# Kernel optimization log

Measured on AMD Instinct MI355X. Metric: run time of the kernel, lower is better.

The kernel has to match this reference:

```python
import jax, jax.numpy as jnp
import numpy as np

N_NODES = 50000
N_EDGES = 800000
IN_DIM = 256     # state_size
HID = 256        # hidden_dim
ACT = 64         # action_size


def gcn_conv(x, src, dst, norm, W, b):
    # PyG GCNConv: out[dst] += norm_e * (x @ W)[src]; then + bias
    h = x @ W                               # [N, out]
    msg = h[src] * norm[:, None]            # [E+N, out]
    agg = jax.ops.segment_sum(msg, dst, num_segments=N_NODES)
    return agg + b


def gcn_norm(edge_index):
    # add self-loops, symmetric normalization deg^-1/2[src]*deg^-1/2[dst]
    loops = jnp.arange(N_NODES, dtype=edge_index.dtype)
    src = jnp.concatenate([edge_index[0], loops])
    dst = jnp.concatenate([edge_index[1], loops])
    deg = jax.ops.segment_sum(jnp.ones_like(dst, dtype=jnp.float32), dst,
                              num_segments=N_NODES)
    dinv = jnp.where(deg > 0, jax.lax.rsqrt(deg), 0.0)
    norm = dinv[src] * dinv[dst]            # [E+N]
    return src, dst, norm


def setup_inputs() -> dict:
    key = jax.random.key(0)
    ks = jax.random.split(key, 12)
    x = jax.random.normal(ks[0], (N_NODES, IN_DIM), dtype=jnp.float32)
    edge_index = jax.random.randint(ks[1], (2, N_EDGES), 0, N_NODES, dtype=jnp.int64)

    def glorot(k, shape):
        lim = float(np.sqrt(6.0 / (shape[0] + shape[1])))
        return jax.random.uniform(k, shape, jnp.float32, -lim, lim)

    return {
        "x": x, "edge_index": edge_index,
        "W1": glorot(ks[2], (IN_DIM, HID)), "b1": jnp.zeros((HID,), jnp.float32),
        "W2": glorot(ks[3], (HID, HID)),    "b2": jnp.zeros((HID,), jnp.float32),
        "fcW1": glorot(ks[4], (HID, HID)),  "fcb1": jnp.zeros((HID,), jnp.float32),
        "fcW2": glorot(ks[5], (HID, HID)),  "fcb2": jnp.zeros((HID,), jnp.float32),
        "fcW3": glorot(ks[6], (HID, ACT)),  "fcb3": jnp.zeros((ACT,), jnp.float32),
    }


def reference(x, edge_index, W1, b1, W2, b2, fcW1, fcb1, fcW2, fcb2, fcW3, fcb3):
    src, dst, norm = gcn_norm(edge_index)
    h = jax.nn.relu(gcn_conv(x, src, dst, norm, W1, b1))   # GNNLayer 1
    h = jax.nn.relu(gcn_conv(h, src, dst, norm, W2, b2))   # GNNLayer 2
    g = jax.nn.relu(jnp.mean(h, axis=0)[None, :])          # [1, HID]
    g = jax.nn.relu(g @ fcW1 + fcb1)
    g = jax.nn.relu(g @ fcW2 + fcb2)
    return g @ fcW3 + fcb3                                 # [1, ACT]
```

## Files before the change

### kernel.cpp

```cpp
#include <hip/hip_runtime.h>

#define N_NODES 50000
#define N_EDGES 800000
#define DIM 256
#define ACT 64
#define SCAN_B 256
#define SCAN_NB ((N_NODES + SCAN_B - 1) / SCAN_B)
#define SLICE_ELEMS ((size_t)N_NODES * 32)
#define AGG_CHUNKS 512
#define TOTAL_GROUPS (AGG_CHUNKS * 32)
#define CSR_MAX (N_EDGES + 16 * N_NODES + 64)
#define NBINS 16
#define NBB (NBINS * SCAN_NB)

typedef __attribute__((ext_vector_type(8))) short short8_t;
typedef __attribute__((ext_vector_type(4))) float f32x4;
typedef __attribute__((ext_vector_type(4))) unsigned short ushort4_t;

__device__ __forceinline__ unsigned short f2b(float x) {
    unsigned u = __float_as_uint(x);
    unsigned r = u + 0x7FFFu + ((u >> 16) & 1u);
    return (unsigned short)(r >> 16);
}

__device__ __forceinline__ int deg_bin_desc(int deg) {
    int rounds = ((deg + 16) & ~15) >> 4;
    if (rounds > NBINS - 1) rounds = NBINS - 1;
    return (NBINS - 1) - rounds;
}


__global__ __launch_bounds__(256) void k_cvt_wt2(const float* __restrict__ W1,
                                                 const float* __restrict__ W2,
                                                 unsigned short* __restrict__ W1t,
                                                 unsigned short* __restrict__ W2t) {
    int b = blockIdx.x;
    const float* W = (b < 256) ? W1 : W2;
    unsigned short* Wt = (b < 256) ? W1t : W2t;
    int i = (b & 255) * 256 + threadIdx.x;
    int k = i >> 8, n = i & 255;
    Wt[n * DIM + k] = f2b(W[k * DIM + n]);
}


__global__ void k_deg_count(const int* __restrict__ ei, int* degi) {
    int e = blockIdx.x * blockDim.x + threadIdx.x;
    if (e < N_EDGES) atomicAdd(&degi[ei[N_EDGES + e]], 1);
}


__global__ __launch_bounds__(256) void k_hist_rank(const int* __restrict__ degi,
                                                   int* blockbin,
                                                   unsigned char* lrank) {
    __shared__ int lh[NBINS];
    int t = threadIdx.x;
    if (t < NBINS) lh[t] = 0;
    __syncthreads();
    int i = blockIdx.x * 256 + t;
    if (i < N_NODES) {
        int bin = deg_bin_desc(degi[i]);
        lrank[i] = (unsigned char)atomicAdd(&lh[bin], 1);
    }
    __syncthreads();
    if (t < NBINS) blockbin[t * SCAN_NB + blockIdx.x] = lh[t];
}

__global__ __launch_bounds__(256) void k_scan_bins(const int* __restrict__ blockbin,
                                                   int* blockbase) {
    __shared__ int sm[256];
    int t = threadIdx.x;
    const int CH = (NBB + 255) / 256;
    int s0 = t * CH;
    int s1 = s0 + CH; if (s1 > NBB) s1 = NBB;
    int s = 0;
    for (int i = s0; i < s1; ++i) s += blockbin[i];
    sm[t] = s;
    __syncthreads();
#pragma unroll
    for (int off = 1; off < 256; off <<= 1) {
        int u = (t >= off) ? sm[t - off] : 0;
        __syncthreads();
        sm[t] += u;
        __syncthreads();
    }
    int base = sm[t] - s;
    for (int i = s0; i < s1; ++i) { int v = blockbin[i]; blockbase[i] = base; base += v; }
}

__global__ __launch_bounds__(256) void k_perm_apply(const int* __restrict__ degi,
                                                    const int* __restrict__ blockbase,
                                                    const unsigned char* __restrict__ lrank,
                                                    int* perm) {
    int i = blockIdx.x * 256 + threadIdx.x;
    if (i >= N_NODES) return;
    int bin = deg_bin_desc(degi[i]);
    perm[blockbase[bin * SCAN_NB + blockIdx.x] + lrank[i]] = i;
}


__global__ __launch_bounds__(SCAN_B) void k_scan_local(const int* __restrict__ degi,
                                                       const int* __restrict__ perm,
                                                       int* lexc, int* btot) {
    __shared__ int sm[SCAN_B];
    int t = threadIdx.x;
    int i = blockIdx.x * SCAN_B + t;
    int v = (i < N_NODES) ? ((degi[perm[i]] + 16) & ~15) : 0;
    sm[t] = v;
    __syncthreads();
#pragma unroll
    for (int off = 1; off < SCAN_B; off <<= 1) {
        int u = (t >= off) ? sm[t - off] : 0;
        __syncthreads();
        sm[t] += u;
        __syncthreads();
    }
    if (i < N_NODES) lexc[i] = sm[t] - v;
    if (t == SCAN_B - 1) btot[blockIdx.x] = sm[t];
}

__global__ __launch_bounds__(SCAN_B) void k_scan_tops(const int* __restrict__ btot,
                                                      int* bbase, int* rowstart) {
    __shared__ int sm[SCAN_B];
    int t = threadIdx.x;
    int v = (t < SCAN_NB) ? btot[t] : 0;
    sm[t] = v;
    __syncthreads();
#pragma unroll
    for (int off = 1; off < SCAN_B; off <<= 1) {
        int u = (t >= off) ? sm[t - off] : 0;
        __syncthreads();
        sm[t] += u;
        __syncthreads();
    }
    if (t < SCAN_NB) bbase[t] = sm[t] - v;
    if (t == SCAN_NB - 1) rowstart[N_NODES] = sm[t];
}

__global__ __launch_bounds__(SCAN_B) void k_scan_apply(const int* __restrict__ degi,
                                                       const int* __restrict__ perm,
                                                       const int* __restrict__ lexc,
                                                       const int* __restrict__ bbase,
                                                       int* rowstart, int* fillpos,
                                                       float* dinv, unsigned* csr4) {
    int i = blockIdx.x * SCAN_B + threadIdx.x;
    if (i >= N_NODES) return;
    int rs = bbase[blockIdx.x] + lexc[i];
    rowstart[i] = rs;
    int n = perm[i];
    int d = degi[n] + 1;
    float di = rsqrtf((float)d);
    dinv[n] = di;
    csr4[rs] = ((unsigned)n << 16) | f2b(di * di);
    fillpos[n] = rs + 1;
}

__global__ void k_fill_edge(const int* __restrict__ ei,
                            const float* __restrict__ dinv, int* fillpos,
                            unsigned* csr4) {
    int e = blockIdx.x * blockDim.x + threadIdx.x;
    if (e < N_EDGES) {
        int s = ei[e];
        int d = ei[N_EDGES + e];
        int p = atomicAdd(&fillpos[d], 1);
        csr4[p] = ((unsigned)s << 16) | f2b(dinv[s] * dinv[d]);
    }
}


template <int AFP32>
__global__ __launch_bounds__(512) void k_gemm_mfma(const void* __restrict__ Ap,
                                                   const unsigned short* __restrict__ Wt,
                                                   unsigned short* __restrict__ H,
                                                   int M) {
    __shared__ char lds[49152];
    char* AsB = lds;
    char* BsB = lds + 16384;

    int tid = threadIdx.x;
    int w = tid >> 6;
    int l = tid & 63;
    int wr = w >> 2, wc = w & 3;
    int r0 = blockIdx.x * 128;

    f32x4 acc[4][4];
#pragma unroll
    for (int i = 0; i < 4; ++i)
#pragma unroll
        for (int j = 0; j < 4; ++j) acc[i][j] = (f32x4)(0.f);

    for (int kt = 0; kt < 4; ++kt) {
        int k0 = kt * 64;
#pragma unroll
        for (int i = 0; i < 2; ++i) {
            int c = tid + i * 512;
            int row = c >> 3, kc = c & 7;
            int gg = r0 + row; if (gg >= M) gg = M - 1;
            short8_t v;
            if (AFP32) {
                const float* A = (const float*)Ap;
                const float4* src = (const float4*)(A + (size_t)gg * DIM + k0 + kc * 8);
                float4 f0 = src[0], f1 = src[1];
                v[0] = (short)f2b(f0.x); v[1] = (short)f2b(f0.y);
                v[2] = (short)f2b(f0.z); v[3] = (short)f2b(f0.w);
                v[4] = (short)f2b(f1.x); v[5] = (short)f2b(f1.y);
                v[6] = (short)f2b(f1.z); v[7] = (short)f2b(f1.w);
            } else {
                const unsigned short* A = (const unsigned short*)Ap;
                int k = k0 + kc * 8;
                int slice = k >> 5, within = k & 31;
                v = *(const short8_t*)(A + (size_t)slice * SLICE_ELEMS + (size_t)gg * 32 + within);
            }
            int off = (row * 128 + kc * 16) ^ ((row & 7) << 4);
            *(short8_t*)(AsB + off) = v;
        }
#pragma unroll
        for (int i = 0; i < 4; ++i) {
            int c = tid + i * 512;
            int n = c >> 3, kc = c & 7;
            short8_t v = *(const short8_t*)(Wt + n * DIM + k0 + kc * 8);
            int off = (n * 128 + kc * 16) ^ ((n & 7) << 4);
            *(short8_t*)(BsB + off) = v;
        }
        __syncthreads();

#pragma unroll
        for (int kf = 0; kf < 2; ++kf) {
            int kb = kf * 64 + (l >> 4) * 16;
            short8_t a[4], b[4];
#pragma unroll
            for (int fm = 0; fm < 4; ++fm) {
                int ra = wr * 64 + fm * 16 + (l & 15);
                a[fm] = *(const short8_t*)(AsB + ((ra * 128 + kb) ^ ((ra & 7) << 4)));
            }
#pragma unroll
            for (int fn = 0; fn < 4; ++fn) {
                int nb = wc * 64 + fn * 16 + (l & 15);
                b[fn] = *(const short8_t*)(BsB + ((nb * 128 + kb) ^ ((nb & 7) << 4)));
            }
#pragma unroll
            for (int fm = 0; fm < 4; ++fm)
#pragma unroll
                for (int fn = 0; fn < 4; ++fn)
                    acc[fm][fn] = __builtin_amdgcn_mfma_f32_16x16x32_bf16(
                        a[fm], b[fn], acc[fm][fn], 0, 0, 0);
        }
        __syncthreads();
    }

#pragma unroll
    for (int fm = 0; fm < 4; ++fm) {
#pragma unroll
        for (int i = 0; i < 4; ++i) {
            int row = r0 + wr * 64 + fm * 16 + ((l >> 4) << 2) + i;
            if (row >= M) continue;
#pragma unroll
            for (int fn = 0; fn < 4; ++fn) {
                int col = wc * 64 + fn * 16 + (l & 15);
                int slice = col >> 5;
                H[(size_t)slice * SLICE_ELEMS + (size_t)row * 32 + (col & 31)] = f2b(acc[fm][fn][i]);
            }
        }
    }
}


__global__ __launch_bounds__(256) void k_agg_sliced(const unsigned short* __restrict__ H,
                                                    const int* __restrict__ rowstart,
                                                    const unsigned* __restrict__ csr4,
                                                    const int* __restrict__ perm,
                                                    const float* __restrict__ bias,
                                                    unsigned short* __restrict__ X,
                                                    float* __restrict__ gsum,
                                                    int write_out) {
    __shared__ unsigned pbuf[32 * 68];
    int slice = blockIdx.x & 7;
    int chunk = blockIdx.x >> 3;
    int g = threadIdx.x >> 3;
    int lane = threadIdx.x & 7;
    const char* Hb = (const char*)(H + (size_t)slice * SLICE_ELEMS) + (lane << 3);
    unsigned short* Xs = X + (size_t)slice * SLICE_ELEMS;
    int d0 = slice * 32 + lane * 4;
    float4 bb = *(const float4*)&bias[d0];
    float c0 = 0.f, c1 = 0.f, c2 = 0.f, c3 = 0.f;
    unsigned* ps = pbuf + g * 68;
    int fg = chunk * 32 + g;
    for (int idx = fg; idx < N_NODES; idx += TOTAL_GROUPS) {
        int n = perm[idx];
        int beg = rowstart[idx], end = rowstart[idx + 1];
        float a0 = 0.f, a1 = 0.f, a2 = 0.f, a3 = 0.f;
        uint4 u = *(const uint4*)(csr4 + beg + (lane << 2));
        int r = 0;
        for (int e = beg; e < end; e += 32, ++r) {
            int en = (e + 32 < end) ? e + 32 : e;
            uint4 un = *(const uint4*)(csr4 + en + (lane << 2));
            unsigned* pb = ps + (r & 1) * 32;
            *(uint4*)(pb + (lane << 2)) = u;
#pragma unroll
            for (int s = 0; s < 2; ++s) {
                if (e + (s << 4) >= end) break;
                unsigned pp[16];
#pragma unroll
                for (int i = 0; i < 16; ++i) pp[i] = pb[(s << 4) + i];
                uint2 q[16];
#pragma unroll
                for (int i = 0; i < 16; ++i)
                    q[i] = *(const uint2*)(Hb + ((pp[i] >> 16) << 6));
#pragma unroll
                for (int i = 0; i < 16; ++i) {
                    float nm = __uint_as_float(pp[i] << 16);
                    a0 = fmaf(nm, __uint_as_float(q[i].x << 16), a0);
                    a1 = fmaf(nm, __uint_as_float(q[i].x & 0xFFFF0000u), a1);
                    a2 = fmaf(nm, __uint_as_float(q[i].y << 16), a2);
                    a3 = fmaf(nm, __uint_as_float(q[i].y & 0xFFFF0000u), a3);
                }
            }
            u = un;
        }
        float o0 = fmaxf(a0 + bb.x, 0.f);
        float o1 = fmaxf(a1 + bb.y, 0.f);
        float o2 = fmaxf(a2 + bb.z, 0.f);
        float o3 = fmaxf(a3 + bb.w, 0.f);
        if (write_out) {
            ushort4_t o; o.x = f2b(o0); o.y = f2b(o1); o.z = f2b(o2); o.w = f2b(o3);
            *(ushort4_t*)(Xs + (size_t)n * 32 + (lane << 2)) = o;
        }
        c0 += o0; c1 += o1; c2 += o2; c3 += o3;
    }
    if (gsum) {
        __shared__ float4 smr[256];
        int tid = threadIdx.x;
        smr[tid] = make_float4(c0, c1, c2, c3);
        __syncthreads();
#pragma unroll
        for (int off = 128; off >= 8; off >>= 1) {
            if (tid < off) {
                float4 a = smr[tid], b = smr[tid + off];
                smr[tid] = make_float4(a.x + b.x, a.y + b.y, a.z + b.z, a.w + b.w);
            }
            __syncthreads();
        }
        if (tid < 8) {
            float4 v = smr[tid];
            atomicAdd(&gsum[d0], v.x);
            atomicAdd(&gsum[d0 + 1], v.y);
            atomicAdd(&gsum[d0 + 2], v.z);
            atomicAdd(&gsum[d0 + 3], v.w);
        }
    }
}


template <int STRIDE, int RELU_IN, int RELU_OUT>
__global__ __launch_bounds__(256) void k_fcx(const float* __restrict__ gin,
                                             const float* __restrict__ W,
                                             const float* __restrict__ bias,
                                             float* __restrict__ gout,
                                             float scale) {
    __shared__ float red[16][17];
    int t = threadIdx.x;
    int lo = t & 15;
    int o = blockIdx.x * 16 + lo;
    int kc = t >> 4;
    float acc = 0.f;
#pragma unroll
    for (int i = 0; i < 16; ++i) {
        int k = kc * 16 + i;
        float gv = gin[k] * scale;
        if (RELU_IN) gv = fmaxf(gv, 0.f);
        acc = fmaf(gv, W[k * STRIDE + o], acc);
    }
    red[kc][lo] = acc;
    __syncthreads();
    if (t < 16) {
        float s = bias[blockIdx.x * 16 + t];
#pragma unroll
        for (int j = 0; j < 16; ++j) s += red[j][t];
        if (RELU_OUT) s = fmaxf(s, 0.f);
        gout[blockIdx.x * 16 + t] = s;
    }
}


extern "C" void kernel_launch(void* const* d_in, const int* in_sizes, int n_in,
                              void* d_out, int out_size, void* d_ws, size_t ws_size,
                              hipStream_t stream) {
    const float* x    = (const float*)d_in[0];
    const int*   ei   = (const int*)d_in[1];
    const float* W1   = (const float*)d_in[2];
    const float* b1   = (const float*)d_in[3];
    const float* W2   = (const float*)d_in[4];
    const float* b2   = (const float*)d_in[5];
    const float* fcW1 = (const float*)d_in[6];
    const float* fcb1 = (const float*)d_in[7];
    const float* fcW2 = (const float*)d_in[8];
    const float* fcb2 = (const float*)d_in[9];
    const float* fcW3 = (const float*)d_in[10];
    const float* fcb3 = (const float*)d_in[11];
    float* out = (float*)d_out;

    char* w = (char*)d_ws;
    size_t o = 0;
#define CARVE(name, type, count) \
    type* name = (type*)(w + o); \
    o += (((size_t)(count) * sizeof(type)) + 255) & ~(size_t)255;
    CARVE(degi, int, N_NODES)
    CARVE(gsum, float, DIM)
    CARVE(rowstart, int, N_NODES + 1)
    CARVE(fillpos, int, N_NODES)
    CARVE(dinv, float, N_NODES)
    CARVE(lexc, int, N_NODES)
    CARVE(btot, int, SCAN_NB)
    CARVE(bbase, int, SCAN_NB)
    CARVE(blockbin, int, NBB)
    CARVE(blockbase, int, NBB)
    CARVE(perm, int, N_NODES)
    CARVE(lrank, unsigned char, N_NODES)
    CARVE(csr4, unsigned, CSR_MAX)
    CARVE(g1, float, DIM)
    CARVE(g2, float, DIM)
    CARVE(W1t, unsigned short, DIM * DIM)
    CARVE(W2t, unsigned short, DIM * DIM)
    CARVE(Hbuf, unsigned short, (size_t)N_NODES * DIM)
    CARVE(Xbuf, unsigned short, (size_t)N_NODES * DIM)
#undef CARVE

    hipMemsetAsync(degi, 0, (size_t)((char*)rowstart - (char*)degi), stream);
    hipMemsetAsync(csr4, 0, (size_t)CSR_MAX * sizeof(unsigned), stream);

    k_cvt_wt2<<<512, 256, 0, stream>>>(W1, W2, W1t, W2t);

    k_deg_count<<<(N_EDGES + 255) / 256, 256, 0, stream>>>(ei, degi);
    k_hist_rank<<<SCAN_NB, 256, 0, stream>>>(degi, blockbin, lrank);
    k_scan_bins<<<1, 256, 0, stream>>>(blockbin, blockbase);
    k_perm_apply<<<SCAN_NB, 256, 0, stream>>>(degi, blockbase, lrank, perm);
    k_scan_local<<<SCAN_NB, SCAN_B, 0, stream>>>(degi, perm, lexc, btot);
    k_scan_tops<<<1, SCAN_B, 0, stream>>>(btot, bbase, rowstart);
    k_scan_apply<<<SCAN_NB, SCAN_B, 0, stream>>>(degi, perm, lexc, bbase, rowstart,
                                                 fillpos, dinv, csr4);
    k_fill_edge<<<(N_EDGES + 255) / 256, 256, 0, stream>>>(ei, dinv, fillpos, csr4);

    int gemm_grid = (N_NODES + 127) / 128;
    k_gemm_mfma<1><<<gemm_grid, 512, 0, stream>>>(x, W1t, Hbuf, N_NODES);
    k_agg_sliced<<<8 * AGG_CHUNKS, 256, 0, stream>>>(Hbuf, rowstart, csr4, perm, b1,
                                                     Xbuf, (float*)nullptr, 1);
    k_gemm_mfma<0><<<gemm_grid, 512, 0, stream>>>(Xbuf, W2t, Hbuf, N_NODES);
    k_agg_sliced<<<8 * AGG_CHUNKS, 256, 0, stream>>>(Hbuf, rowstart, csr4, perm, b2,
                                                     Xbuf, gsum, 0);

    k_fcx<DIM, 1, 1><<<16, 256, 0, stream>>>(gsum, fcW1, fcb1, g1, 1.0f / (float)N_NODES);
    k_fcx<DIM, 0, 1><<<16, 256, 0, stream>>>(g1, fcW2, fcb2, g2, 1.0f);
    k_fcx<ACT, 0, 0><<<4, 256, 0, stream>>>(g2, fcW3, fcb3, out, 1.0f);
}
```

Before: 266.6 us.

## Pre-swizzle weights, use direct global-to-LDS loads, and fold CSR scans into bin math

The weight conversion kernel now writes W1/W2 in bf16, pre-swizzled into the exact LDS tile layout. The GEMM can then stage B tiles, and the bf16 A tiles of the second layer, with global_load_lds DMA instead of register round-trips. The first aggregation now writes its output row-major rather than sliced, so the second GEMM can load it contiguously. The multi-kernel CSR row-start scan (scan_local/tops/apply) is replaced by closed-form offsets computed per degree bin, because every row in a bin has the same padded length. This removes three kernel launches and several intermediate buffers, at the cost of padding rows to their bin's maximum length and making the aggregation's writes strided by the slice layout.

```diff
diff --git a/kernel.cpp b/kernel.cpp
--- a/kernel.cpp
+++ b/kernel.cpp
@@ -29,17 +29,29 @@
     return (NBINS - 1) - rounds;
 }
 
+__device__ __forceinline__ void gload_lds16(const void* g, void* l) {
+    __builtin_amdgcn_global_load_lds(
+        (const __attribute__((address_space(1))) void*)g,
+        (__attribute__((address_space(3))) void*)l, 16, 0, 0);
+}
+
 
 __global__ __launch_bounds__(256) void k_cvt_wt2(const float* __restrict__ W1,
                                                  const float* __restrict__ W2,
-                                                 unsigned short* __restrict__ W1t,
-                                                 unsigned short* __restrict__ W2t) {
+                                                 unsigned short* __restrict__ W1s,
+                                                 unsigned short* __restrict__ W2s) {
     int b = blockIdx.x;
-    const float* W = (b < 256) ? W1 : W2;
-    unsigned short* Wt = (b < 256) ? W1t : W2t;
-    int i = (b & 255) * 256 + threadIdx.x;
-    int k = i >> 8, n = i & 255;
-    Wt[n * DIM + k] = f2b(W[k * DIM + n]);
+    const float* W = (b < 32) ? W1 : W2;
+    unsigned short* Ws = (b < 32) ? W1s : W2s;
+    int c = (b & 31) * 256 + threadIdx.x;
+    int kt = c >> 11, cc = c & 2047;
+    int n = cc >> 3;
+    int kc = (cc & 7) ^ (n & 7);
+    int kbase = kt * 64 + kc * 8;
+    short8_t v;
+#pragma unroll
+    for (int j = 0; j < 8; ++j) v[j] = (short)f2b(W[(kbase + j) * DIM + n]);
+    *(short8_t*)(Ws + (size_t)c * 8) = v;
 }
 
 
@@ -66,7 +78,8 @@
 }
 
 __global__ __launch_bounds__(256) void k_scan_bins(const int* __restrict__ blockbin,
-                                                   int* blockbase) {
+                                                   int* blockbase, int* binfo,
+                                                   int* rowstart) {
     __shared__ int sm[256];
     int t = threadIdx.x;
     const int CH = (NBB + 255) / 256;
@@ -85,73 +98,43 @@
     }
     int base = sm[t] - s;
     for (int i = s0; i < s1; ++i) { int v = blockbin[i]; blockbase[i] = base; base += v; }
-}
-
-__global__ __launch_bounds__(256) void k_perm_apply(const int* __restrict__ degi,
-                                                    const int* __restrict__ blockbase,
-                                                    const unsigned char* __restrict__ lrank,
-                                                    int* perm) {
+    __syncthreads();
+    if (t == 0) {
+        int cacc = 0;
+#pragma unroll
+        for (int b = 0; b < NBINS; ++b) {
+            int bs = blockbase[b * SCAN_NB];
+            int bend = (b == NBINS - 1) ? N_NODES : blockbase[(b + 1) * SCAN_NB];
+            binfo[b] = bs;
+            binfo[NBINS + 1 + b] = cacc;
+            cacc += (bend - bs) * (16 * (NBINS - 1 - b));
+        }
+        binfo[NBINS] = N_NODES;
+        rowstart[N_NODES] = cacc;
+    }
+}
+
+__global__ __launch_bounds__(256) void k_perm_scatter(const int* __restrict__ degi,
+                                                      const int* __restrict__ blockbase,
+                                                      const int* __restrict__ binfo,
+                                                      const unsigned char* __restrict__ lrank,
+                                                      int* perm, int* rowstart,
+                                                      int* fillpos, float* dinv,
+                                                      unsigned* csr4) {
     int i = blockIdx.x * 256 + threadIdx.x;
     if (i >= N_NODES) return;
-    int bin = deg_bin_desc(degi[i]);
-    perm[blockbase[bin * SCAN_NB + blockIdx.x] + lrank[i]] = i;
-}
-
-
-__global__ __launch_bounds__(SCAN_B) void k_scan_local(const int* __restrict__ degi,
-                                                       const int* __restrict__ perm,
-                                                       int* lexc, int* btot) {
-    __shared__ int sm[SCAN_B];
-    int t = threadIdx.x;
-    int i = blockIdx.x * SCAN_B + t;
-    int v = (i < N_NODES) ? ((degi[perm[i]] + 16) & ~15) : 0;
-    sm[t] = v;
-    __syncthreads();
-#pragma unroll
-    for (int off = 1; off < SCAN_B; off <<= 1) {
-        int u = (t >= off) ? sm[t - off] : 0;
-        __syncthreads();
-        sm[t] += u;
-        __syncthreads();
-    }
-    if (i < N_NODES) lexc[i] = sm[t] - v;
-    if (t == SCAN_B - 1) btot[blockIdx.x] = sm[t];
-}
-
-__global__ __launch_bounds__(SCAN_B) void k_scan_tops(const int* __restrict__ btot,
-                                                      int* bbase, int* rowstart) {
-    __shared__ int sm[SCAN_B];
-    int t = threadIdx.x;
-    int v = (t < SCAN_NB) ? btot[t] : 0;
-    sm[t] = v;
-    __syncthreads();
-#pragma unroll
-    for (int off = 1; off < SCAN_B; off <<= 1) {
-        int u = (t >= off) ? sm[t - off] : 0;
-        __syncthreads();
-        sm[t] += u;
-        __syncthreads();
-    }
-    if (t < SCAN_NB) bbase[t] = sm[t] - v;
-    if (t == SCAN_NB - 1) rowstart[N_NODES] = sm[t];
-}
-
-__global__ __launch_bounds__(SCAN_B) void k_scan_apply(const int* __restrict__ degi,
-                                                       const int* __restrict__ perm,
-                                                       const int* __restrict__ lexc,
-                                                       const int* __restrict__ bbase,
-                                                       int* rowstart, int* fillpos,
-                                                       float* dinv, unsigned* csr4) {
-    int i = blockIdx.x * SCAN_B + threadIdx.x;
-    if (i >= N_NODES) return;
-    int rs = bbase[blockIdx.x] + lexc[i];
-    rowstart[i] = rs;
-    int n = perm[i];
-    int d = degi[n] + 1;
+    int deg = degi[i];
+    int bin = deg_bin_desc(deg);
+    int pos = blockbase[bin * SCAN_NB + blockIdx.x] + lrank[i];
+    perm[pos] = i;
+    int plen = 16 * (NBINS - 1 - bin);
+    int rs = binfo[NBINS + 1 + bin] + (pos - binfo[bin]) * plen;
+    rowstart[pos] = rs;
+    int d = deg + 1;
     float di = rsqrtf((float)d);
-    dinv[n] = di;
-    csr4[rs] = ((unsigned)n << 16) | f2b(di * di);
-    fillpos[n] = rs + 1;
+    dinv[i] = di;
+    csr4[rs] = ((unsigned)i << 16) | f2b(di * di);
+    fillpos[i] = rs + 1;
 }
 
 __global__ void k_fill_edge(const int* __restrict__ ei,
@@ -169,7 +152,7 @@
 
 template <int AFP32>
 __global__ __launch_bounds__(512) void k_gemm_mfma(const void* __restrict__ Ap,
-                                                   const unsigned short* __restrict__ Wt,
+                                                   const unsigned short* __restrict__ WtS,
                                                    unsigned short* __restrict__ H,
                                                    int M) {
     __shared__ char lds[49152];
@@ -190,36 +173,42 @@
 
     for (int kt = 0; kt < 4; ++kt) {
         int k0 = kt * 64;
-#pragma unroll
-        for (int i = 0; i < 2; ++i) {
-            int c = tid + i * 512;
-            int row = c >> 3, kc = c & 7;
-            int gg = r0 + row; if (gg >= M) gg = M - 1;
-            short8_t v;
-            if (AFP32) {
-                const float* A = (const float*)Ap;
+        if (AFP32) {
+            const float* A = (const float*)Ap;
+#pragma unroll
+            for (int i = 0; i < 2; ++i) {
+                int c = tid + i * 512;
+                int row = c >> 3, kc = c & 7;
+                int gg = r0 + row; if (gg >= M) gg = M - 1;
                 const float4* src = (const float4*)(A + (size_t)gg * DIM + k0 + kc * 8);
                 float4 f0 = src[0], f1 = src[1];
+                short8_t v;
                 v[0] = (short)f2b(f0.x); v[1] = (short)f2b(f0.y);
                 v[2] = (short)f2b(f0.z); v[3] = (short)f2b(f0.w);
                 v[4] = (short)f2b(f1.x); v[5] = (short)f2b(f1.y);
                 v[6] = (short)f2b(f1.z); v[7] = (short)f2b(f1.w);
-            } else {
-                const unsigned short* A = (const unsigned short*)Ap;
-                int k = k0 + kc * 8;
-                int slice = k >> 5, within = k & 31;
-                v = *(const short8_t*)(A + (size_t)slice * SLICE_ELEMS + (size_t)gg * 32 + within);
-            }
-            int off = (row * 128 + kc * 16) ^ ((row & 7) << 4);
-            *(short8_t*)(AsB + off) = v;
-        }
-#pragma unroll
-        for (int i = 0; i < 4; ++i) {
-            int c = tid + i * 512;
-            int n = c >> 3, kc = c & 7;
-            short8_t v = *(const short8_t*)(Wt + n * DIM + k0 + kc * 8);
-            int off = (n * 128 + kc * 16) ^ ((n & 7) << 4);
-            *(short8_t*)(BsB + off) = v;
+                int off = (row * 128 + kc * 16) ^ ((row & 7) << 4);
+                *(short8_t*)(AsB + off) = v;
+            }
+        } else {
+            const char* Arm = (const char*)Ap;
+#pragma unroll
+            for (int i = 0; i < 2; ++i) {
+                int s = w * 2 + i;
+                int c = s * 64 + l;
+                int row = c >> 3;
+                int kc = (c & 7) ^ (row & 7);
+                int gg = r0 + row; if (gg >= M) gg = M - 1;
+                gload_lds16(Arm + (size_t)gg * 512 + k0 * 2 + kc * 16, AsB + s * 1024);
+            }
+        }
+        {
+            const char* Bsrc = (const char*)WtS + (size_t)kt * 32768;
+#pragma unroll
+            for (int i = 0; i < 4; ++i) {
+                int s = w * 4 + i;
+                gload_lds16(Bsrc + s * 1024 + l * 16, BsB + s * 1024);
+            }
         }
         __syncthreads();
 
@@ -278,7 +267,6 @@
     int g = threadIdx.x >> 3;
     int lane = threadIdx.x & 7;
     const char* Hb = (const char*)(H + (size_t)slice * SLICE_ELEMS) + (lane << 3);
-    unsigned short* Xs = X + (size_t)slice * SLICE_ELEMS;
     int d0 = slice * 32 + lane * 4;
     float4 bb = *(const float4*)&bias[d0];
     float c0 = 0.f, c1 = 0.f, c2 = 0.f, c3 = 0.f;
@@ -322,7 +310,7 @@
         float o3 = fmaxf(a3 + bb.w, 0.f);
         if (write_out) {
             ushort4_t o; o.x = f2b(o0); o.y = f2b(o1); o.z = f2b(o2); o.w = f2b(o3);
-            *(ushort4_t*)(Xs + (size_t)n * 32 + (lane << 2)) = o;
+            *(ushort4_t*)(X + (size_t)n * DIM + slice * 32 + (lane << 2)) = o;
         }
         c0 += o0; c1 += o1; c2 += o2; c3 += o3;
     }
@@ -408,18 +396,16 @@
     CARVE(rowstart, int, N_NODES + 1)
     CARVE(fillpos, int, N_NODES)
     CARVE(dinv, float, N_NODES)
-    CARVE(lexc, int, N_NODES)
-    CARVE(btot, int, SCAN_NB)
-    CARVE(bbase, int, SCAN_NB)
     CARVE(blockbin, int, NBB)
     CARVE(blockbase, int, NBB)
+    CARVE(binfo, int, 2 * NBINS + 2)
     CARVE(perm, int, N_NODES)
     CARVE(lrank, unsigned char, N_NODES)
     CARVE(csr4, unsigned, CSR_MAX)
     CARVE(g1, float, DIM)
     CARVE(g2, float, DIM)
-    CARVE(W1t, unsigned short, DIM * DIM)
-    CARVE(W2t, unsigned short, DIM * DIM)
+    CARVE(W1s, unsigned short, DIM * DIM)
+    CARVE(W2s, unsigned short, DIM * DIM)
     CARVE(Hbuf, unsigned short, (size_t)N_NODES * DIM)
     CARVE(Xbuf, unsigned short, (size_t)N_NODES * DIM)
 #undef CARVE
@@ -427,23 +413,20 @@
     hipMemsetAsync(degi, 0, (size_t)((char*)rowstart - (char*)degi), stream);
     hipMemsetAsync(csr4, 0, (size_t)CSR_MAX * sizeof(unsigned), stream);
 
-    k_cvt_wt2<<<512, 256, 0, stream>>>(W1, W2, W1t, W2t);
+    k_cvt_wt2<<<64, 256, 0, stream>>>(W1, W2, W1s, W2s);
 
     k_deg_count<<<(N_EDGES + 255) / 256, 256, 0, stream>>>(ei, degi);
     k_hist_rank<<<SCAN_NB, 256, 0, stream>>>(degi, blockbin, lrank);
-    k_scan_bins<<<1, 256, 0, stream>>>(blockbin, blockbase);
-    k_perm_apply<<<SCAN_NB, 256, 0, stream>>>(degi, blockbase, lrank, perm);
-    k_scan_local<<<SCAN_NB, SCAN_B, 0, stream>>>(degi, perm, lexc, btot);
-    k_scan_tops<<<1, SCAN_B, 0, stream>>>(btot, bbase, rowstart);
-    k_scan_apply<<<SCAN_NB, SCAN_B, 0, stream>>>(degi, perm, lexc, bbase, rowstart,
-                                                 fillpos, dinv, csr4);
+    k_scan_bins<<<1, 256, 0, stream>>>(blockbin, blockbase, binfo, rowstart);
+    k_perm_scatter<<<SCAN_NB, 256, 0, stream>>>(degi, blockbase, binfo, lrank,
+                                                perm, rowstart, fillpos, dinv, csr4);
     k_fill_edge<<<(N_EDGES + 255) / 256, 256, 0, stream>>>(ei, dinv, fillpos, csr4);
 
     int gemm_grid = (N_NODES + 127) / 128;
-    k_gemm_mfma<1><<<gemm_grid, 512, 0, stream>>>(x, W1t, Hbuf, N_NODES);
+    k_gemm_mfma<1><<<gemm_grid, 512, 0, stream>>>(x, W1s, Hbuf, N_NODES);
     k_agg_sliced<<<8 * AGG_CHUNKS, 256, 0, stream>>>(Hbuf, rowstart, csr4, perm, b1,
                                                      Xbuf, (float*)nullptr, 1);
-    k_gemm_mfma<0><<<gemm_grid, 512, 0, stream>>>(Xbuf, W2t, Hbuf, N_NODES);
+    k_gemm_mfma<0><<<gemm_grid, 512, 0, stream>>>(Xbuf, W2s, Hbuf, N_NODES);
     k_agg_sliced<<<8 * AGG_CHUNKS, 256, 0, stream>>>(Hbuf, rowstart, csr4, perm, b2,
                                                      Xbuf, gsum, 0);
 
```

Measured after the change: 255.2 us. -4.3%, faster.
